# Kernel tuning notes

Measured on AMD Instinct MI355X. Metric: run time of the kernel, lower is better.

Reference implementation:

```python
import jax, jax.numpy as jnp
import numpy as np

N_SRNA = 20000
N_MRNA = 100000
HID = 128
E_S2M = 1_000_000
E_M2M = 2_000_000
E_LBL = 500_000
N_LAYERS = 2


def setup_inputs() -> dict:
    key = jax.random.key(0)
    ks = jax.random.split(key, 20)
    s = 0.05
    inp = {
        # edge lists (rev edge types are flips, derived inside reference)
        "s2m_src": jax.random.randint(ks[0], (E_S2M,), 0, N_SRNA),
        "s2m_dst": jax.random.randint(ks[1], (E_S2M,), 0, N_MRNA),
        "m2m_src": jax.random.randint(ks[2], (E_M2M,), 0, N_MRNA),
        "m2m_dst": jax.random.randint(ks[3], (E_M2M,), 0, N_MRNA),
        "label_src": jax.random.randint(ks[4], (E_LBL,), 0, N_SRNA),
        "label_dst": jax.random.randint(ks[5], (E_LBL,), 0, N_MRNA),
        # embeddings (node_id is arange over all nodes -> identity lookup)
        "srna_emb": jax.random.normal(ks[6], (N_SRNA, HID), jnp.float32),
        "mrna_emb": jax.random.normal(ks[7], (N_MRNA, HID), jnp.float32),
        # per-layer stacked params. SAGEConv: out = lin_l(mean_agg)+lin_r(x_dst)
        "sage_s2m_Wl": jax.random.normal(ks[8], (N_LAYERS, HID, HID), jnp.float32) * s,
        "sage_s2m_bl": jnp.zeros((N_LAYERS, HID), jnp.float32),
        "sage_s2m_Wr": jax.random.normal(ks[9], (N_LAYERS, HID, HID), jnp.float32) * s,
        "sage_rev_Wl": jax.random.normal(ks[10], (N_LAYERS, HID, HID), jnp.float32) * s,
        "sage_rev_bl": jnp.zeros((N_LAYERS, HID), jnp.float32),
        "sage_rev_Wr": jax.random.normal(ks[11], (N_LAYERS, HID, HID), jnp.float32) * s,
        # GCNConv: out = propagate(norm, x @ W) + b
        "gcn_m2m_W": jax.random.normal(ks[12], (N_LAYERS, HID, HID), jnp.float32) * s,
        "gcn_m2m_b": jnp.zeros((N_LAYERS, HID), jnp.float32),
        "gcn_rev_W": jax.random.normal(ks[13], (N_LAYERS, HID, HID), jnp.float32) * s,
        "gcn_rev_b": jnp.zeros((N_LAYERS, HID), jnp.float32),
    }
    return inp


def _sage(x_src, x_dst, src, dst, n_dst, Wl, bl, Wr):
    # PyG SAGEConv (aggr='mean', root_weight=True): lin_l(mean_msg) + lin_r(x_dst)
    agg = jax.ops.segment_sum(x_src[src], dst, num_segments=n_dst)  # [n_dst, h]
    cnt = jax.ops.segment_sum(jnp.ones((src.shape[0],), x_src.dtype), dst,
                              num_segments=n_dst)
    agg = agg / jnp.maximum(cnt, 1.0)[:, None]
    return agg @ Wl + bl + x_dst @ Wr


def _gcn(x, src, dst, n, W, b):
    # PyG GCNConv: add self-loops, sym-normalize, x @ W, propagate, + bias
    xw = x @ W  # [n, h]
    deg = jax.ops.segment_sum(jnp.ones((src.shape[0],), x.dtype), dst,
                              num_segments=n) + 1.0  # +1 self-loop
    dinv = jax.lax.rsqrt(deg)
    norm = dinv[src] * dinv[dst]  # [E]
    out = jax.ops.segment_sum(norm[:, None] * xw[src], dst, num_segments=n)
    out = out + (dinv * dinv)[:, None] * xw  # self-loop term
    return out + b


def reference(s2m_src, s2m_dst, m2m_src, m2m_dst, label_src, label_dst,
              srna_emb, mrna_emb,
              sage_s2m_Wl, sage_s2m_bl, sage_s2m_Wr,
              sage_rev_Wl, sage_rev_bl, sage_rev_Wr,
              gcn_m2m_W, gcn_m2m_b, gcn_rev_W, gcn_rev_b):
    x_s, x_m = srna_emb, mrna_emb
    for l in range(N_LAYERS):
        # HeteroConv aggr='sum' over edge types per dst node type
        m_new = _sage(x_s, x_m, s2m_src, s2m_dst, N_MRNA,
                      sage_s2m_Wl[l], sage_s2m_bl[l], sage_s2m_Wr[l])
        m_new = m_new + _gcn(x_m, m2m_src, m2m_dst, N_MRNA,
                             gcn_m2m_W[l], gcn_m2m_b[l])
        m_new = m_new + _gcn(x_m, m2m_dst, m2m_src, N_MRNA,
                             gcn_rev_W[l], gcn_rev_b[l])  # rev_similar = flip
        s_new = _sage(x_m, x_s, s2m_dst, s2m_src, N_SRNA,
                      sage_rev_Wl[l], sage_rev_bl[l], sage_rev_Wr[l])
        x_s, x_m = jax.nn.relu(s_new), jax.nn.relu(m_new)
    # Classifier: dot product over labeled (srna, mrna) pairs
    return (x_s[label_src] * x_m[label_dst]).sum(axis=-1)
```

## Files before the change

### kernel.cpp

```cpp
#include <hip/hip_runtime.h>
#include <hip/hip_fp16.h>

#define NS 20000
#define NM 100000
#define H  128
#define ES 1000000
#define EM 2000000
#define EL 500000

#define SH_M 7
#define SH_S 6
#define NB_SD 782
#define NB_SS 313
#define NB_MD 782
#define NB_MS 782
#define CAP_SD 1664
#define CAP_SS 3904
#define CAP_MD 3200
#define CAP_MS 3200
#define MAXCAP 3904
#define CHUNK 4096
#define B_SD ((ES + CHUNK - 1) / CHUNK)
#define B_SS ((ES + CHUNK - 1) / CHUNK)
#define B_MD ((EM + CHUNK - 1) / CHUNK)
#define B_MS ((EM + CHUNK - 1) / CHUNK)
#define VAL_MASK 0x1FFFF

#define MB_M (NM / 16)
#define MB_S (NS / 16)
#define APAD 136

#define PB_M 12500
#define PB_S 2500
#define PB_W 768
#define PB_F 391

typedef _Float16 half8 __attribute__((ext_vector_type(8)));
typedef float floatx4 __attribute__((ext_vector_type(4)));

__global__ __launch_bounds__(256) void place1_sorted(
        const int* __restrict__ s2m_src, const int* __restrict__ s2m_dst,
        const int* __restrict__ m2m_src, const int* __restrict__ m2m_dst,
        int* __restrict__ bc,
        unsigned int* __restrict__ p_sd, unsigned int* __restrict__ p_ss,
        unsigned int* __restrict__ p_md, unsigned int* __restrict__ p_ms) {
    __shared__ unsigned int rec[CHUNK];
    __shared__ unsigned short eb[CHUNK];
    __shared__ int cnt[1024];
    __shared__ int gbase[1024];

    int b = blockIdx.x;
    const int *keys, *vals; int shift, cap, E, bcoff; unsigned int* pp;
    int cb;
    if (b < B_SD)                    { cb = b;                      keys = s2m_dst; vals = s2m_src; shift = SH_M; cap = CAP_SD; E = ES; bcoff = 0;     pp = p_sd; }
    else if (b < B_SD+B_SS)          { cb = b - B_SD;               keys = s2m_src; vals = s2m_dst; shift = SH_S; cap = CAP_SS; E = ES; bcoff = 16384; pp = p_ss; }
    else if (b < B_SD+B_SS+B_MD)     { cb = b - B_SD - B_SS;        keys = m2m_dst; vals = m2m_src; shift = SH_M; cap = CAP_MD; E = EM; bcoff = 32768; pp = p_md; }
    else                             { cb = b - B_SD - B_SS - B_MD; keys = m2m_src; vals = m2m_dst; shift = SH_M; cap = CAP_MS; E = EM; bcoff = 49152; pp = p_ms; }
    int* bcp = bc + bcoff;

    int t = threadIdx.x;
    int e0 = cb * CHUNK;
    int nv = E - e0; if (nv > CHUNK) nv = CHUNK;

    for (int i = t; i < nv; i += 256) {
        int k = keys[e0 + i];
        int v = vals[e0 + i];
        int bkt = k >> shift;
        rec[i] = ((unsigned int)(k - (bkt << shift)) << 17) | (unsigned int)v;
        eb[i] = (unsigned short)bkt;
    }
#pragma unroll
    for (int j = 0; j < 4; ++j) cnt[t * 4 + j] = 0;
    __syncthreads();
    for (int i = t; i < nv; i += 256) atomicAdd(&cnt[eb[i]], 1);
    __syncthreads();
#pragma unroll
    for (int j = 0; j < 4; ++j) {
        int bk = t * 4 + j;
        int c = cnt[bk];
        if (c > 0) {
            gbase[bk] = atomicAdd(&bcp[bk << 4], c);
            cnt[bk] = 0;
        }
    }
    __syncthreads();
    for (int i = t; i < nv; i += 256) {
        int bk = eb[i];
        int pos = atomicAdd(&cnt[bk], 1);
        int o = gbase[bk] + pos;
        if (o < cap) pp[(size_t)bk * cap + o] = rec[i];
    }
}

__global__ __launch_bounds__(256) void place2_fused(
        const int* __restrict__ bc,
        const unsigned int* __restrict__ p_sd, const unsigned int* __restrict__ p_ss,
        const unsigned int* __restrict__ p_md, const unsigned int* __restrict__ p_ms,
        int* __restrict__ adj_sd, int* __restrict__ adj_ss,
        int* __restrict__ adj_md, int* __restrict__ adj_ms,
        int* __restrict__ off_sd, int* __restrict__ off_ss,
        int* __restrict__ off_md, int* __restrict__ off_ms,
        int* __restrict__ cnt_sd, int* __restrict__ cnt_ss,
        int* __restrict__ cnt_md, int* __restrict__ cnt_ms) {
    __shared__ unsigned int lp[MAXCAP];
    __shared__ int hist[128], cur[128], sbuf[128];
    int b = blockIdx.x;
    int c, lb;
    if (b < NB_SD)                    { c = 0; lb = b; }
    else if (b < NB_SD+NB_SS)         { c = 1; lb = b - NB_SD; }
    else if (b < NB_SD+NB_SS+NB_MD)   { c = 2; lb = b - NB_SD - NB_SS; }
    else                              { c = 3; lb = b - NB_SD - NB_SS - NB_MD; }
    const unsigned int* pp; int *adj, *offp, *cntp; int shift, cap, n;
    switch (c) {
    case 0:  pp = p_sd; adj = adj_sd; offp = off_sd; cntp = cnt_sd; shift = SH_M; cap = CAP_SD; n = NM; break;
    case 1:  pp = p_ss; adj = adj_ss; offp = off_ss; cntp = cnt_ss; shift = SH_S; cap = CAP_SS; n = NS; break;
    case 2:  pp = p_md; adj = adj_md; offp = off_md; cntp = cnt_md; shift = SH_M; cap = CAP_MD; n = NM; break;
    default: pp = p_ms; adj = adj_ms; offp = off_ms; cntp = cnt_ms; shift = SH_M; cap = CAP_MS; n = NM; break;
    }
    int t = threadIdx.x;
    int k = bc[c * 16384 + (lb << 4)];
    if (k > cap) k = cap;
    int base = lb << shift;
    int npb = 1 << shift;
    int bb = lb * cap;
    for (int i = t; i < k; i += 256) lp[i] = pp[(size_t)lb * cap + i];
    if (t < npb) hist[t] = 0;
    __syncthreads();
    for (int i = t; i < k; i += 256) atomicAdd(&hist[lp[i] >> 17], 1);
    __syncthreads();
    int v = (t < npb) ? hist[t] : 0;
    if (t < 128) sbuf[t] = v;
    __syncthreads();
    for (int d = 1; d < 128; d <<= 1) {
        int x = 0;
        if (t >= d && t < 128) x = sbuf[t - d];
        __syncthreads();
        if (t >= d && t < 128) sbuf[t] += x;
        __syncthreads();
    }
    if (t < npb) {
        int excl = sbuf[t] - v;
        cur[t] = excl;
        int node = base + t;
        if (node < n) { offp[node] = bb + excl; cntp[node] = v; }
    }
    __syncthreads();
    for (int i = t; i < k; i += 256) {
        unsigned int p = lp[i];
        int pos = atomicAdd(&cur[p >> 17], 1);
        adj[(size_t)bb + pos] = (int)(p & VAL_MASK);
    }
}

__global__ __launch_bounds__(256) void prep_all(
        const float* __restrict__ m_emb, const float* __restrict__ s_emb,
        const float* __restrict__ w0, const float* __restrict__ w1,
        const float* __restrict__ w2, const float* __restrict__ w3,
        const float* __restrict__ w4, const float* __restrict__ w5,
        const int* __restrict__ c_md, const int* __restrict__ c_ms,
        __half* __restrict__ xm16, __half* __restrict__ xs16,
        __half* __restrict__ wbuf, float* __restrict__ dvf, float* __restrict__ dvr) {
    int b = blockIdx.x;
    int t = threadIdx.x;
    if (b < PB_M) {
        long long i = (long long)b * 256 + t;
        float4 v = *(const float4*)&m_emb[i * 4];
        __half2 h0 = __floats2half2_rn(v.x, v.y);
        __half2 h1 = __floats2half2_rn(v.z, v.w);
        __half2* o = (__half2*)&xm16[i * 4];
        o[0] = h0; o[1] = h1;
    } else if (b < PB_M + PB_S) {
        long long i = (long long)(b - PB_M) * 256 + t;
        float4 v = *(const float4*)&s_emb[i * 4];
        __half2 h0 = __floats2half2_rn(v.x, v.y);
        __half2 h1 = __floats2half2_rn(v.z, v.w);
        __half2* o = (__half2*)&xs16[i * 4];
        o[0] = h0; o[1] = h1;
    } else if (b < PB_M + PB_S + PB_W) {
        int idx = (b - PB_M - PB_S) * 256 + t;
        int mat = idx / (H * H);
        int rem = idx % (H * H);
        int n = rem / H;
        int k = rem % H;
        const float* base;
        switch (mat >> 1) {
        case 0: base = w0; break; case 1: base = w1; break; case 2: base = w2; break;
        case 3: base = w3; break; case 4: base = w4; break; default: base = w5; break;
        }
        base += (size_t)(mat & 1) * H * H;
        wbuf[(size_t)mat * H * H + (size_t)n * H + k] = __float2half(base[(size_t)k * H + n]);
    } else {
        int i = (b - PB_M - PB_S - PB_W) * 256 + t;
        if (i < NM) {
            dvf[i] = rsqrtf((float)c_md[i] + 1.0f);
            dvr[i] = rsqrtf((float)c_ms[i] + 1.0f);
        }
    }
}

__device__ __forceinline__ void gacc_plain(const __half* __restrict__ X,
                                           const int* __restrict__ adj,
                                           int o, int k, int c, float (&acc)[8]) {
    int j = 0;
    for (; j + 8 <= k; j += 8) {
        int s0 = adj[o+j+0], s1 = adj[o+j+1], s2 = adj[o+j+2], s3 = adj[o+j+3];
        int s4 = adj[o+j+4], s5 = adj[o+j+5], s6 = adj[o+j+6], s7 = adj[o+j+7];
        half8 v0 = *(const half8*)(X + (size_t)s0 * H + c);
        half8 v1 = *(const half8*)(X + (size_t)s1 * H + c);
        half8 v2 = *(const half8*)(X + (size_t)s2 * H + c);
        half8 v3 = *(const half8*)(X + (size_t)s3 * H + c);
        half8 v4 = *(const half8*)(X + (size_t)s4 * H + c);
        half8 v5 = *(const half8*)(X + (size_t)s5 * H + c);
        half8 v6 = *(const half8*)(X + (size_t)s6 * H + c);
        half8 v7 = *(const half8*)(X + (size_t)s7 * H + c);
#pragma unroll
        for (int i = 0; i < 8; ++i)
            acc[i] += (float)v0[i] + (float)v1[i] + (float)v2[i] + (float)v3[i]
                    + (float)v4[i] + (float)v5[i] + (float)v6[i] + (float)v7[i];
    }
    for (; j + 4 <= k; j += 4) {
        int s0 = adj[o+j+0], s1 = adj[o+j+1], s2 = adj[o+j+2], s3 = adj[o+j+3];
        half8 v0 = *(const half8*)(X + (size_t)s0 * H + c);
        half8 v1 = *(const half8*)(X + (size_t)s1 * H + c);
        half8 v2 = *(const half8*)(X + (size_t)s2 * H + c);
        half8 v3 = *(const half8*)(X + (size_t)s3 * H + c);
#pragma unroll
        for (int i = 0; i < 8; ++i)
            acc[i] += (float)v0[i] + (float)v1[i] + (float)v2[i] + (float)v3[i];
    }
    for (; j < k; ++j) {
        int s = adj[o + j];
        half8 v = *(const half8*)(X + (size_t)s * H + c);
#pragma unroll
        for (int i = 0; i < 8; ++i) acc[i] += (float)v[i];
    }
}

__device__ __forceinline__ void gacc_weighted(const __half* __restrict__ X,
                                              const int* __restrict__ adj,
                                              const float* __restrict__ dinv,
                                              int o, int k, int c, float (&acc)[8]) {
    int j = 0;
    for (; j + 8 <= k; j += 8) {
        int s0 = adj[o+j+0], s1 = adj[o+j+1], s2 = adj[o+j+2], s3 = adj[o+j+3];
        int s4 = adj[o+j+4], s5 = adj[o+j+5], s6 = adj[o+j+6], s7 = adj[o+j+7];
        float d0 = dinv[s0], d1 = dinv[s1], d2 = dinv[s2], d3 = dinv[s3];
        float d4 = dinv[s4], d5 = dinv[s5], d6 = dinv[s6], d7 = dinv[s7];
        half8 v0 = *(const half8*)(X + (size_t)s0 * H + c);
        half8 v1 = *(const half8*)(X + (size_t)s1 * H + c);
        half8 v2 = *(const half8*)(X + (size_t)s2 * H + c);
        half8 v3 = *(const half8*)(X + (size_t)s3 * H + c);
        half8 v4 = *(const half8*)(X + (size_t)s4 * H + c);
        half8 v5 = *(const half8*)(X + (size_t)s5 * H + c);
        half8 v6 = *(const half8*)(X + (size_t)s6 * H + c);
        half8 v7 = *(const half8*)(X + (size_t)s7 * H + c);
#pragma unroll
        for (int i = 0; i < 8; ++i)
            acc[i] += d0 * (float)v0[i] + d1 * (float)v1[i] + d2 * (float)v2[i] + d3 * (float)v3[i]
                    + d4 * (float)v4[i] + d5 * (float)v5[i] + d6 * (float)v6[i] + d7 * (float)v7[i];
    }
    for (; j + 4 <= k; j += 4) {
        int s0 = adj[o+j+0], s1 = adj[o+j+1], s2 = adj[o+j+2], s3 = adj[o+j+3];
        float d0 = dinv[s0], d1 = dinv[s1], d2 = dinv[s2], d3 = dinv[s3];
        half8 v0 = *(const half8*)(X + (size_t)s0 * H + c);
        half8 v1 = *(const half8*)(X + (size_t)s1 * H + c);
        half8 v2 = *(const half8*)(X + (size_t)s2 * H + c);
        half8 v3 = *(const half8*)(X + (size_t)s3 * H + c);
#pragma unroll
        for (int i = 0; i < 8; ++i)
            acc[i] += d0 * (float)v0[i] + d1 * (float)v1[i] + d2 * (float)v2[i] + d3 * (float)v3[i];
    }
    for (; j < k; ++j) {
        int s = adj[o + j];
        float ds = dinv[s];
        half8 v = *(const half8*)(X + (size_t)s * H + c);
#pragma unroll
        for (int i = 0; i < 8; ++i) acc[i] += ds * (float)v[i];
    }
}

__device__ __forceinline__ void st_h8(__half* p, const float (&a)[8]) {
    half8 h;
#pragma unroll
    for (int i = 0; i < 8; ++i) h[i] = (_Float16)a[i];
    *(half8*)p = h;
}

__global__ __launch_bounds__(256) void sage_sd(
        const __half* __restrict__ xs_in,
        const int* __restrict__ off_sd, const int* __restrict__ cnt_sd,
        const int* __restrict__ adj_sd,
        __half* __restrict__ SA) {
    long long gid = (long long)blockIdx.x * 256 + threadIdx.x;
    int g = (int)(gid >> 4);
    int c = ((int)gid & 15) * 8;
    float acc[8] = {0.f,0.f,0.f,0.f,0.f,0.f,0.f,0.f};
    int k = cnt_sd[g];
    gacc_plain(xs_in, adj_sd, off_sd[g], k, c, acc);
    float ic = 1.0f / fmaxf((float)k, 1.0f);
#pragma unroll
    for (int i = 0; i < 8; ++i) acc[i] *= ic;
    st_h8(SA + (size_t)g * H + c, acc);
}

__global__ __launch_bounds__(256) void fused_layer(
        const __half* __restrict__ xs_in, const __half* __restrict__ xm_in,
        const __half* __restrict__ SA,
        const int* __restrict__ off_md, const int* __restrict__ cnt_md, const int* __restrict__ adj_md,
        const int* __restrict__ off_ms, const int* __restrict__ cnt_ms, const int* __restrict__ adj_ms,
        const int* __restrict__ off_ss, const int* __restrict__ cnt_ss, const int* __restrict__ adj_ss,
        const float* __restrict__ dvf, const float* __restrict__ dvr,
        const __half* __restrict__ wbuf,
        const float* __restrict__ bl, const float* __restrict__ gb,
        const float* __restrict__ grb, const float* __restrict__ bls,
        __half* __restrict__ xm_out, __half* __restrict__ xs_out, int layer)
{
    __shared__ __half At[4][16][APAD];
    const int t = threadIdx.x;
    const int grp = t >> 4;
    const int c = (t & 15) * 8;
    const size_t HH = (size_t)H * H;
    const bool isM = (int)blockIdx.x < MB_M;

    if (isM) {
        const int r = blockIdx.x * 16 + grp;
        *(half8*)&At[0][grp][c] = *(const half8*)(SA + (size_t)r * H + c);
        half8 self = *(const half8*)(xm_in + (size_t)r * H + c);
        *(half8*)&At[1][grp][c] = self;
        float acc[8] = {0.f,0.f,0.f,0.f,0.f,0.f,0.f,0.f};
        gacc_weighted(xm_in, adj_md, dvf, off_md[r], cnt_md[r], c, acc);
        float dd = dvf[r], s2 = dd * dd;
#pragma unroll
        for (int i = 0; i < 8; ++i) acc[i] = dd * acc[i] + s2 * (float)self[i];
        st_h8(&At[2][grp][c], acc);
#pragma unroll
        for (int i = 0; i < 8; ++i) acc[i] = 0.f;
        gacc_weighted(xm_in, adj_ms, dvr, off_ms[r], cnt_ms[r], c, acc);
        dd = dvr[r]; s2 = dd * dd;
#pragma unroll
        for (int i = 0; i < 8; ++i) acc[i] = dd * acc[i] + s2 * (float)self[i];
        st_h8(&At[3][grp][c], acc);
        __syncthreads();
        const int w = t >> 6, lane = t & 63, quad = lane >> 4, nlo = lane & 15;
        floatx4 o0, o1;
        o0[0]=0.f;o0[1]=0.f;o0[2]=0.f;o0[3]=0.f;
        o1[0]=0.f;o1[1]=0.f;o1[2]=0.f;o1[3]=0.f;
        const int t0 = 2 * w, t1 = 2 * w + 1;
#pragma unroll
        for (int seg = 0; seg < 4; ++seg) {
            const __half* Wt = wbuf + (size_t)(seg * 2 + layer) * HH;
#pragma unroll
            for (int k0 = 0; k0 < 128; k0 += 32) {
                half8 a = *(const half8*)&At[seg][nlo][k0 + quad * 8];
                half8 b0 = *(const half8*)(Wt + (size_t)(t0 * 16 + nlo) * H + k0 + quad * 8);
                half8 b1 = *(const half8*)(Wt + (size_t)(t1 * 16 + nlo) * H + k0 + quad * 8);
                o0 = __builtin_amdgcn_mfma_f32_16x16x32_f16(a, b0, o0, 0, 0, 0);
                o1 = __builtin_amdgcn_mfma_f32_16x16x32_f16(a, b1, o1, 0, 0, 0);
            }
        }
        const int bm = blockIdx.x * 16;
#pragma unroll
        for (int u = 0; u < 2; ++u) {
            floatx4 oo = u ? o1 : o0;
            int col = (2 * w + u) * 16 + nlo;
            float bias = bl[col] + gb[col] + grb[col];
#pragma unroll
            for (int i = 0; i < 4; ++i) {
                int rr = bm + quad * 4 + i;
                xm_out[(size_t)rr * H + col] = __float2half(fmaxf(oo[i] + bias, 0.f));
            }
        }
    } else {
        const int blk = (int)blockIdx.x - MB_M;
        const int r = blk * 16 + grp;
        float acc[8] = {0.f,0.f,0.f,0.f,0.f,0.f,0.f,0.f};
        int k = cnt_ss[r];
        gacc_plain(xm_in, adj_ss, off_ss[r], k, c, acc);
        float ic = 1.0f / fmaxf((float)k, 1.0f);
#pragma unroll
        for (int i = 0; i < 8; ++i) acc[i] *= ic;
        st_h8(&At[0][grp][c], acc);
        *(half8*)&At[1][grp][c] = *(const half8*)(xs_in + (size_t)r * H + c);
        __syncthreads();
        const int w = t >> 6, lane = t & 63, quad = lane >> 4, nlo = lane & 15;
        floatx4 o0, o1;
        o0[0]=0.f;o0[1]=0.f;o0[2]=0.f;o0[3]=0.f;
        o1[0]=0.f;o1[1]=0.f;o1[2]=0.f;o1[3]=0.f;
        const int t0 = 2 * w, t1 = 2 * w + 1;
#pragma unroll
        for (int seg = 0; seg < 2; ++seg) {
            const __half* Wt = wbuf + (size_t)((4 + seg) * 2 + layer) * HH;
#pragma unroll
            for (int k0 = 0; k0 < 128; k0 += 32) {
                half8 a = *(const half8*)&At[seg][nlo][k0 + quad * 8];
                half8 b0 = *(const half8*)(Wt + (size_t)(t0 * 16 + nlo) * H + k0 + quad * 8);
                half8 b1 = *(const half8*)(Wt + (size_t)(t1 * 16 + nlo) * H + k0 + quad * 8);
                o0 = __builtin_amdgcn_mfma_f32_16x16x32_f16(a, b0, o0, 0, 0, 0);
                o1 = __builtin_amdgcn_mfma_f32_16x16x32_f16(a, b1, o1, 0, 0, 0);
            }
        }
        const int bm = blk * 16;
#pragma unroll
        for (int u = 0; u < 2; ++u) {
            floatx4 oo = u ? o1 : o0;
            int col = (2 * w + u) * 16 + nlo;
            float bias = bls[col];
#pragma unroll
            for (int i = 0; i < 4; ++i) {
                int rr = bm + quad * 4 + i;
                xs_out[(size_t)rr * H + col] = __float2half(fmaxf(oo[i] + bias, 0.f));
            }
        }
    }
}

__device__ __forceinline__ float4 ldh4(const __half* __restrict__ X, long long idx) {
    float2 raw = *(const float2*)(X + idx);
    __half2 h0 = *(__half2*)&raw.x;
    __half2 h1 = *(__half2*)&raw.y;
    float2 fa = __half22float2(h0);
    float2 fb = __half22float2(h1);
    return make_float4(fa.x, fa.y, fb.x, fb.y);
}

__global__ void classify(const __half* __restrict__ xs16, const __half* __restrict__ xm16,
                         const int* __restrict__ ls, const int* __restrict__ ld,
                         float* __restrict__ out, int P) {
    long long gid = (long long)blockIdx.x * blockDim.x + threadIdx.x;
    int p = (int)(gid >> 5);
    if (p >= P) return;
    int lane = (int)gid & 31;
    int a = ls[p], b = ld[p];
    float4 u = ldh4(xs16, (long long)a * H + lane * 4);
    float4 v = ldh4(xm16, (long long)b * H + lane * 4);
    float s = u.x * v.x + u.y * v.y + u.z * v.z + u.w * v.w;
    for (int off = 16; off > 0; off >>= 1) s += __shfl_down(s, off, 32);
    if (lane == 0) out[p] = s;
}

extern "C" void kernel_launch(void* const* d_in, const int* in_sizes, int n_in,
                              void* d_out, int out_size, void* d_ws, size_t ws_size,
                              hipStream_t stream) {
    const int* s2m_src = (const int*)d_in[0];
    const int* s2m_dst = (const int*)d_in[1];
    const int* m2m_src = (const int*)d_in[2];
    const int* m2m_dst = (const int*)d_in[3];
    const int* lbl_src = (const int*)d_in[4];
    const int* lbl_dst = (const int*)d_in[5];
    const float* s_emb = (const float*)d_in[6];
    const float* m_emb = (const float*)d_in[7];
    const float* Wl_s2m = (const float*)d_in[8];
    const float* bl_s2m = (const float*)d_in[9];
    const float* Wr_s2m = (const float*)d_in[10];
    const float* Wl_rev = (const float*)d_in[11];
    const float* bl_rev = (const float*)d_in[12];
    const float* Wr_rev = (const float*)d_in[13];
    const float* gW  = (const float*)d_in[14];
    const float* gb  = (const float*)d_in[15];
    const float* grW = (const float*)d_in[16];
    const float* grb = (const float*)d_in[17];

    __half* hws = (__half*)d_ws;
    size_t ho = 0;
    __half* xm16_a = hws + ho; ho += (size_t)NM * H;
    __half* xm16_b = hws + ho; ho += (size_t)NM * H;
    __half* xs16_a = hws + ho; ho += (size_t)NS * H;
    __half* xs16_b = hws + ho; ho += (size_t)NS * H;
    __half* scratch = hws + ho; ho += (size_t)(3 * NM + NS) * H;
    __half* wbuf = hws + ho; ho += (size_t)12 * H * H;

    float* fws = (float*)(hws + ho);
    size_t fo = 0;
    float* dvf = fws + fo; fo += NM;
    float* dvr = fws + fo; fo += NM;

    int* ip = (int*)(fws + fo);
    size_t io = 0;
    int* off_sd = ip + io; io += NM;
    int* off_ss = ip + io; io += NS;
    int* off_md = ip + io; io += NM;
    int* off_ms = ip + io; io += NM;
    int* cnt_sd = ip + io; io += NM;
    int* cnt_ss = ip + io; io += NS;
    int* cnt_md = ip + io; io += NM;
    int* cnt_ms = ip + io; io += NM;
    int* bc     = ip + io; io += 4 * 16384;
    int* adj_sd = ip + io; io += NB_SD * CAP_SD;
    int* adj_ss = ip + io; io += NB_SS * CAP_SS;
    int* adj_md = ip + io; io += NB_MD * CAP_MD;
    int* adj_ms = ip + io; io += NB_MS * CAP_MS;

    unsigned int* p_sd = (unsigned int*)scratch;
    unsigned int* p_ss = p_sd + (size_t)NB_SD * CAP_SD;
    unsigned int* p_md = p_ss + (size_t)NB_SS * CAP_SS;
    unsigned int* p_ms = p_md + (size_t)NB_MD * CAP_MD;

    __half* SA = scratch;

    hipMemsetAsync(bc, 0, 4 * 16384 * sizeof(int), stream);
    place1_sorted<<<B_SD + B_SS + B_MD + B_MS, 256, 0, stream>>>(
        s2m_src, s2m_dst, m2m_src, m2m_dst, bc, p_sd, p_ss, p_md, p_ms);
    place2_fused<<<NB_SD + NB_SS + NB_MD + NB_MS, 256, 0, stream>>>(
        bc, p_sd, p_ss, p_md, p_ms,
        adj_sd, adj_ss, adj_md, adj_ms,
        off_sd, off_ss, off_md, off_ms,
        cnt_sd, cnt_ss, cnt_md, cnt_ms);

    prep_all<<<PB_M + PB_S + PB_W + PB_F, 256, 0, stream>>>(
        m_emb, s_emb, Wl_s2m, Wr_s2m, gW, grW, Wl_rev, Wr_rev,
        cnt_md, cnt_ms, xm16_a, xs16_a, wbuf, dvf, dvr);

    const __half* xin_m = xm16_a;
    const __half* xin_s = xs16_a;
    __half* xout_m = xm16_b;
    __half* xout_s = xs16_b;

    for (int l = 0; l < 2; ++l) {
        const size_t bo = (size_t)l * H;
        sage_sd<<<NM * 16 / 256, 256, 0, stream>>>(
            xin_s, off_sd, cnt_sd, adj_sd, SA);
        fused_layer<<<MB_M + MB_S, 256, 0, stream>>>(
            xin_s, xin_m, SA,
            off_md, cnt_md, adj_md,
            off_ms, cnt_ms, adj_ms,
            off_ss, cnt_ss, adj_ss,
            dvf, dvr, wbuf,
            bl_s2m + bo, gb + bo, grb + bo, bl_rev + bo,
            xout_m, xout_s, l);
        const __half* tm = xin_m; xin_m = xout_m; xout_m = (__half*)tm;
        const __half* ts = xin_s; xin_s = xout_s; xout_s = (__half*)ts;
    }

    classify<<<(int)(((long long)EL * 32 + 255) / 256), 256, 0, stream>>>(
        xin_s, xin_m, lbl_src, lbl_dst, (float*)d_out, EL);
}
```

Baseline: 845.3 us.

## Assign one 16-row tile per wave with wave-local LDS and no block barriers

The fused layer kernel now has each wavefront own a full 16-row tile and compute all 128 output columns with eight MFMA accumulators. Previously a 256-thread block shared one tile across four waves and synchronized with __syncthreads. Each wave stages its inputs segment by segment (self, SA, forward GCN, reverse GCN) into its own LDS slice and runs the MFMA right after each stage, using a lightweight lgkmcnt wait in place of a block barrier. This is meant to remove block-wide sync stalls and let gather latency overlap across independent waves. The cost is more accumulator registers per wave, each lane gathering four rows serially, a reread of self rows, and correctness that rests on the wave-only fence.

```diff
diff --git a/kernel.cpp b/kernel.cpp
--- a/kernel.cpp
+++ b/kernel.cpp
@@ -26,8 +26,9 @@
 #define B_MS ((EM + CHUNK - 1) / CHUNK)
 #define VAL_MASK 0x1FFFF
 
-#define MB_M (NM / 16)
-#define MB_S (NS / 16)
+#define T_M (NM / 16)
+#define T_S (NS / 16)
+#define T_TOT (T_M + T_S)
 #define APAD 136
 
 #define PB_M 12500
@@ -37,6 +38,11 @@
 
 typedef _Float16 half8 __attribute__((ext_vector_type(8)));
 typedef float floatx4 __attribute__((ext_vector_type(4)));
+
+__device__ __forceinline__ void wave_fence() {
+    asm volatile("s_waitcnt lgkmcnt(0)" ::: "memory");
+    __builtin_amdgcn_sched_barrier(0);
+}
 
 __global__ __launch_bounds__(256) void place1_sorted(
         const int* __restrict__ s2m_src, const int* __restrict__ s2m_dst,
@@ -303,6 +309,20 @@
     st_h8(SA + (size_t)g * H + c, acc);
 }
 
+__device__ __forceinline__ void mfma_seg(const __half (*A)[APAD],
+                                         const __half* __restrict__ Wt,
+                                         int nlo, int quad, floatx4 (&acc8)[8]) {
+#pragma unroll
+    for (int k0 = 0; k0 < 128; k0 += 32) {
+        half8 a = *(const half8*)&A[nlo][k0 + quad * 8];
+#pragma unroll
+        for (int t8 = 0; t8 < 8; ++t8) {
+            half8 b = *(const half8*)(Wt + (size_t)(t8 * 16 + nlo) * H + k0 + quad * 8);
+            acc8[t8] = __builtin_amdgcn_mfma_f32_16x16x32_f16(a, b, acc8[t8], 0, 0, 0);
+        }
+    }
+}
+
 __global__ __launch_bounds__(256) void fused_layer(
         const __half* __restrict__ xs_in, const __half* __restrict__ xm_in,
         const __half* __restrict__ SA,
@@ -317,98 +337,103 @@
 {
     __shared__ __half At[4][16][APAD];
     const int t = threadIdx.x;
-    const int grp = t >> 4;
-    const int c = (t & 15) * 8;
+    const int w = t >> 6;
+    const int lane = t & 63;
+    const int quad = lane >> 4;
+    const int nlo = lane & 15;
+    const int rg = lane >> 4;
+    const int c = (lane & 15) * 8;
+    const int tile = (int)blockIdx.x * 4 + w;
     const size_t HH = (size_t)H * H;
-    const bool isM = (int)blockIdx.x < MB_M;
-
-    if (isM) {
-        const int r = blockIdx.x * 16 + grp;
-        *(half8*)&At[0][grp][c] = *(const half8*)(SA + (size_t)r * H + c);
-        half8 self = *(const half8*)(xm_in + (size_t)r * H + c);
-        *(half8*)&At[1][grp][c] = self;
-        float acc[8] = {0.f,0.f,0.f,0.f,0.f,0.f,0.f,0.f};
-        gacc_weighted(xm_in, adj_md, dvf, off_md[r], cnt_md[r], c, acc);
-        float dd = dvf[r], s2 = dd * dd;
-#pragma unroll
-        for (int i = 0; i < 8; ++i) acc[i] = dd * acc[i] + s2 * (float)self[i];
-        st_h8(&At[2][grp][c], acc);
-#pragma unroll
-        for (int i = 0; i < 8; ++i) acc[i] = 0.f;
-        gacc_weighted(xm_in, adj_ms, dvr, off_ms[r], cnt_ms[r], c, acc);
-        dd = dvr[r]; s2 = dd * dd;
-#pragma unroll
-        for (int i = 0; i < 8; ++i) acc[i] = dd * acc[i] + s2 * (float)self[i];
-        st_h8(&At[3][grp][c], acc);
-        __syncthreads();
-        const int w = t >> 6, lane = t & 63, quad = lane >> 4, nlo = lane & 15;
-        floatx4 o0, o1;
-        o0[0]=0.f;o0[1]=0.f;o0[2]=0.f;o0[3]=0.f;
-        o1[0]=0.f;o1[1]=0.f;o1[2]=0.f;o1[3]=0.f;
-        const int t0 = 2 * w, t1 = 2 * w + 1;
-#pragma unroll
-        for (int seg = 0; seg < 4; ++seg) {
-            const __half* Wt = wbuf + (size_t)(seg * 2 + layer) * HH;
-#pragma unroll
-            for (int k0 = 0; k0 < 128; k0 += 32) {
-                half8 a = *(const half8*)&At[seg][nlo][k0 + quad * 8];
-                half8 b0 = *(const half8*)(Wt + (size_t)(t0 * 16 + nlo) * H + k0 + quad * 8);
-                half8 b1 = *(const half8*)(Wt + (size_t)(t1 * 16 + nlo) * H + k0 + quad * 8);
-                o0 = __builtin_amdgcn_mfma_f32_16x16x32_f16(a, b0, o0, 0, 0, 0);
-                o1 = __builtin_amdgcn_mfma_f32_16x16x32_f16(a, b1, o1, 0, 0, 0);
+    __half (*A)[APAD] = At[w];
+
+    floatx4 acc8[8];
+#pragma unroll
+    for (int i = 0; i < 8; ++i) { acc8[i][0]=0.f; acc8[i][1]=0.f; acc8[i][2]=0.f; acc8[i][3]=0.f; }
+
+    if (tile < T_M) {
+        const int base = tile * 16;
+#pragma unroll
+        for (int g = 0; g < 4; ++g) {
+            int r = base + g * 4 + rg;
+            *(half8*)&A[g * 4 + rg][c] = *(const half8*)(xm_in + (size_t)r * H + c);
+        }
+        wave_fence();
+        mfma_seg(A, wbuf + (size_t)(1 * 2 + layer) * HH, nlo, quad, acc8);
+        wave_fence();
+#pragma unroll
+        for (int g = 0; g < 4; ++g) {
+            int r = base + g * 4 + rg;
+            *(half8*)&A[g * 4 + rg][c] = *(const half8*)(SA + (size_t)r * H + c);
+        }
+        wave_fence();
+        mfma_seg(A, wbuf + (size_t)(0 * 2 + layer) * HH, nlo, quad, acc8);
+        wave_fence();
+        for (int g = 0; g < 4; ++g) {
+            int r = base + g * 4 + rg;
+            float acc[8] = {0.f,0.f,0.f,0.f,0.f,0.f,0.f,0.f};
+            gacc_weighted(xm_in, adj_md, dvf, off_md[r], cnt_md[r], c, acc);
+            float dd = dvf[r], s2 = dd * dd;
+            half8 self = *(const half8*)(xm_in + (size_t)r * H + c);
+#pragma unroll
+            for (int i = 0; i < 8; ++i) acc[i] = dd * acc[i] + s2 * (float)self[i];
+            st_h8(&A[g * 4 + rg][c], acc);
+        }
+        wave_fence();
+        mfma_seg(A, wbuf + (size_t)(2 * 2 + layer) * HH, nlo, quad, acc8);
+        wave_fence();
+        for (int g = 0; g < 4; ++g) {
+            int r = base + g * 4 + rg;
+            float acc[8] = {0.f,0.f,0.f,0.f,0.f,0.f,0.f,0.f};
+            gacc_weighted(xm_in, adj_ms, dvr, off_ms[r], cnt_ms[r], c, acc);
+            float dd = dvr[r], s2 = dd * dd;
+            half8 self = *(const half8*)(xm_in + (size_t)r * H + c);
+#pragma unroll
+            for (int i = 0; i < 8; ++i) acc[i] = dd * acc[i] + s2 * (float)self[i];
+            st_h8(&A[g * 4 + rg][c], acc);
+        }
+        wave_fence();
+        mfma_seg(A, wbuf + (size_t)(3 * 2 + layer) * HH, nlo, quad, acc8);
+#pragma unroll
+        for (int t8 = 0; t8 < 8; ++t8) {
+            int col = t8 * 16 + nlo;
+            float bias = bl[col] + gb[col] + grb[col];
+#pragma unroll
+            for (int i = 0; i < 4; ++i) {
+                int rr = base + quad * 4 + i;
+                xm_out[(size_t)rr * H + col] = __float2half(fmaxf(acc8[t8][i] + bias, 0.f));
             }
         }
-        const int bm = blockIdx.x * 16;
-#pragma unroll
-        for (int u = 0; u < 2; ++u) {
-            floatx4 oo = u ? o1 : o0;
-            int col = (2 * w + u) * 16 + nlo;
-            float bias = bl[col] + gb[col] + grb[col];
+    } else {
+        const int base = (tile - T_M) * 16;
+#pragma unroll
+        for (int g = 0; g < 4; ++g) {
+            int r = base + g * 4 + rg;
+            *(half8*)&A[g * 4 + rg][c] = *(const half8*)(xs_in + (size_t)r * H + c);
+        }
+        wave_fence();
+        mfma_seg(A, wbuf + (size_t)(5 * 2 + layer) * HH, nlo, quad, acc8);
+        wave_fence();
+        for (int g = 0; g < 4; ++g) {
+            int r = base + g * 4 + rg;
+            float acc[8] = {0.f,0.f,0.f,0.f,0.f,0.f,0.f,0.f};
+            int k = cnt_ss[r];
+            gacc_plain(xm_in, adj_ss, off_ss[r], k, c, acc);
+            float ic = 1.0f / fmaxf((float)k, 1.0f);
+#pragma unroll
+            for (int i = 0; i < 8; ++i) acc[i] *= ic;
+            st_h8(&A[g * 4 + rg][c], acc);
+        }
+        wave_fence();
+        mfma_seg(A, wbuf + (size_t)(4 * 2 + layer) * HH, nlo, quad, acc8);
+#pragma unroll
+        for (int t8 = 0; t8 < 8; ++t8) {
+            int col = t8 * 16 + nlo;
+            float bias = bls[col];
 #pragma unroll
             for (int i = 0; i < 4; ++i) {
-                int rr = bm + quad * 4 + i;
-                xm_out[(size_t)rr * H + col] = __float2half(fmaxf(oo[i] + bias, 0.f));
-            }
-        }
-    } else {
-        const int blk = (int)blockIdx.x - MB_M;
-        const int r = blk * 16 + grp;
-        float acc[8] = {0.f,0.f,0.f,0.f,0.f,0.f,0.f,0.f};
-        int k = cnt_ss[r];
-        gacc_plain(xm_in, adj_ss, off_ss[r], k, c, acc);
-        float ic = 1.0f / fmaxf((float)k, 1.0f);
-#pragma unroll
-        for (int i = 0; i < 8; ++i) acc[i] *= ic;
-        st_h8(&At[0][grp][c], acc);
-        *(half8*)&At[1][grp][c] = *(const half8*)(xs_in + (size_t)r * H + c);
-        __syncthreads();
-        const int w = t >> 6, lane = t & 63, quad = lane >> 4, nlo = lane & 15;
-        floatx4 o0, o1;
-        o0[0]=0.f;o0[1]=0.f;o0[2]=0.f;o0[3]=0.f;
-        o1[0]=0.f;o1[1]=0.f;o1[2]=0.f;o1[3]=0.f;
-        const int t0 = 2 * w, t1 = 2 * w + 1;
-#pragma unroll
-        for (int seg = 0; seg < 2; ++seg) {
-            const __half* Wt = wbuf + (size_t)((4 + seg) * 2 + layer) * HH;
-#pragma unroll
-            for (int k0 = 0; k0 < 128; k0 += 32) {
-                half8 a = *(const half8*)&At[seg][nlo][k0 + quad * 8];
-                half8 b0 = *(const half8*)(Wt + (size_t)(t0 * 16 + nlo) * H + k0 + quad * 8);
-                half8 b1 = *(const half8*)(Wt + (size_t)(t1 * 16 + nlo) * H + k0 + quad * 8);
-                o0 = __builtin_amdgcn_mfma_f32_16x16x32_f16(a, b0, o0, 0, 0, 0);
-                o1 = __builtin_amdgcn_mfma_f32_16x16x32_f16(a, b1, o1, 0, 0, 0);
-            }
-        }
-        const int bm = blk * 16;
-#pragma unroll
-        for (int u = 0; u < 2; ++u) {
-            floatx4 oo = u ? o1 : o0;
-            int col = (2 * w + u) * 16 + nlo;
-            float bias = bls[col];
-#pragma unroll
-            for (int i = 0; i < 4; ++i) {
-                int rr = bm + quad * 4 + i;
-                xs_out[(size_t)rr * H + col] = __float2half(fmaxf(oo[i] + bias, 0.f));
+                int rr = base + quad * 4 + i;
+                xs_out[(size_t)rr * H + col] = __float2half(fmaxf(acc8[t8][i] + bias, 0.f));
             }
         }
     }
@@ -519,7 +544,7 @@
         const size_t bo = (size_t)l * H;
         sage_sd<<<NM * 16 / 256, 256, 0, stream>>>(
             xin_s, off_sd, cnt_sd, adj_sd, SA);
-        fused_layer<<<MB_M + MB_S, 256, 0, stream>>>(
+        fused_layer<<<T_TOT / 4, 256, 0, stream>>>(
             xin_s, xin_m, SA,
             off_md, cnt_md, adj_md,
             off_ms, cnt_ms, adj_ms,
```

New measurement: 1.199 ms. 41.8% more time.
